# Optimization experiments

Hardware: AMD Instinct MI355X
Metric: run time of the kernel (lower is better)

## Reference

```python
import jax, jax.numpy as jnp
import numpy as np

TAU = 2.0
EPS_G = 1e-10   # gumbel numerical eps
EPS_H = 1e-12   # entropy log eps


def _gumbel(u):
    # u ~ Uniform(0,1) -> standard Gumbel noise
    return -jnp.log(-jnp.log(u + EPS_G) + EPS_G)


def setup_inputs() -> dict:
    key = jax.random.key(0)
    k1, k2, k3, k4 = jax.random.split(key, 4)
    B, T, D, K = 4, 1024, 512, 8192
    x = jax.random.normal(k1, (B, T, D), dtype=jnp.float32)
    codebook = jax.random.normal(k2, (K, D), dtype=jnp.float32)
    u1 = jax.random.uniform(k3, (B * T, K), dtype=jnp.float32)
    u2 = jax.random.uniform(k4, (B * T, K), dtype=jnp.float32)
    return {"x": x, "codebook": codebook, "u1": u1, "u2": u2}


def reference(x, codebook, u1, u2):
    B, T, D = x.shape
    x_flat = x.reshape(-1, D)                                  # (N, D)
    x_sq = jnp.sum(x_flat * x_flat, axis=1, keepdims=True)     # (N, 1)
    c_sq = jnp.sum(codebook * codebook, axis=1)                # (K,)
    xc = x_flat @ codebook.T                                   # (N, K)
    logits = -(x_sq + c_sq - 2.0 * xc)                         # -||x - c||^2

    # soft gumbel-softmax (first independent noise draw)
    probs_soft = jax.nn.softmax((logits + _gumbel(u1)) / TAU, axis=-1)  # (N, K)
    quantized_soft = (probs_soft @ codebook).reshape(B, T, D)

    # hard gumbel-softmax indices (second independent noise draw);
    # argmax of the hard one-hot == argmax of perturbed logits
    indices = jnp.argmax(logits + _gumbel(u2), axis=-1).reshape(B, T)

    codebook_loss = jnp.mean((quantized_soft - jax.lax.stop_gradient(x)) ** 2)
    enc_commitment_loss = jnp.mean((x - jax.lax.stop_gradient(quantized_soft)) ** 2)

    entropy = -jnp.sum(probs_soft * jnp.log(probs_soft + EPS_H), axis=1)  # (N,)
    mean_entropy = jnp.mean(entropy)

    return quantized_soft, indices, codebook_loss, enc_commitment_loss, mean_entropy
```

## Files before the change

kernel.cpp:

```cpp
#include <hip/hip_runtime.h>
#include <math.h>

#define NROWS 4096
#define KCODES 8192
#define DDIM 512
#define IDX_OFF 2097152
#define L0_OFF  2101248
#define L1_OFF  2101249
#define ENT_OFF 2101250
#define ARGMAX_MARGIN 0.05f
#define FIX_CHUNK 256
#define FIX_CPR (KCODES / FIX_CHUNK)

#define TOP2_UPD(v1, k1, v2, k2, h, k)                                 \
    do {                                                               \
        if ((h) > (v1)) { v2 = v1; k2 = k1; v1 = (h); k1 = (k); }      \
        else if ((h) > (v2)) { v2 = (h); k2 = (k); }                   \
    } while (0)

typedef __attribute__((ext_vector_type(8))) short bf16x8;
typedef __attribute__((ext_vector_type(4))) float f32x4;

__device__ __forceinline__ float gumbelfast(float u) {
    float a = __logf(u + 1e-10f);
    float b = __logf(1e-10f - a);
    return -b;
}
__device__ __forceinline__ ushort f2bf(float f) {
    uint u = __float_as_uint(f);
    return (ushort)((u + 0x7FFFu + ((u >> 16) & 1u)) >> 16);
}
__device__ __forceinline__ float bf2f(ushort h) {
    return __uint_as_float(((uint)h) << 16);
}

__device__ __forceinline__ float np_log32(float x) {
    return (float)log((double)x);
}
__device__ __forceinline__ float np_gumbel(float u) {
    float a  = __fadd_rn(u, 1e-10f);
    float la = np_log32(a);
    float b  = __fadd_rn(-la, 1e-10f);
    float lb = np_log32(b);
    return -lb;
}
__device__ float np_sumsq512(const float* __restrict__ a) {
    float blk[4];
    #pragma unroll
    for (int b = 0; b < 4; ++b) {
        const float* p = a + b * 128;
        float r[8];
        #pragma unroll
        for (int j = 0; j < 8; ++j) r[j] = __fmul_rn(p[j], p[j]);
        for (int i = 8; i < 128; i += 8) {
            #pragma unroll
            for (int j = 0; j < 8; ++j)
                r[j] = __fadd_rn(r[j], __fmul_rn(p[i + j], p[i + j]));
        }
        blk[b] = __fadd_rn(__fadd_rn(__fadd_rn(r[0], r[1]), __fadd_rn(r[2], r[3])),
                           __fadd_rn(__fadd_rn(r[4], r[5]), __fadd_rn(r[6], r[7])));
    }
    return __fadd_rn(__fadd_rn(blk[0], blk[1]), __fadd_rn(blk[2], blk[3]));
}

__device__ __forceinline__ float dot4(float4 a, float4 b) {
    return a.x*b.x + a.y*b.y + a.z*b.z + a.w*b.w;
}
__device__ __forceinline__ void fma4(float4& o, float p, float4 c) {
    o.x += p*c.x; o.y += p*c.y; o.z += p*c.z; o.w += p*c.w;
}

__global__ __launch_bounds__(256) void vq_csq(const float* __restrict__ cb,
                                              float* __restrict__ csq,
                                              int* __restrict__ flag_cnt) {
    if (blockIdx.x == 0 && threadIdx.x == 0) flag_cnt[0] = 0;
    int row = blockIdx.x * 256 + threadIdx.x;
    if (row < KCODES) csq[row] = np_sumsq512(cb + (size_t)row * DDIM);
}

__global__ __launch_bounds__(256) void vq_fixup(
        const float* __restrict__ x, const float* __restrict__ cb,
        const float* __restrict__ u2, const float* __restrict__ csq,
        const int* __restrict__ flag_cnt, const int* __restrict__ flag_rows,
        float* __restrict__ out) {
    __shared__ float xrow[DDIM];
    __shared__ float bv[4];
    __shared__ int   bk[4];
    const int n = flag_cnt[0];
    for (int w = blockIdx.x; w < n; w += gridDim.x) {
        const int row = flag_rows[w];
        for (int i = threadIdx.x; i < DDIM; i += 256)
            xrow[i] = x[(size_t)row * DDIM + i];
        __syncthreads();
        const float xsq = np_sumsq512(xrow);
        float best = -1e30f; int bidx = 0x7fffffff;
        for (int k = threadIdx.x; k < KCODES; k += 256) {
            const float* c = cb + (size_t)k * DDIM;
            float acc1 = 0.f, acc2 = 0.f;
            #pragma unroll 8
            for (int d = 0; d < 384; ++d) acc1 = fmaf(xrow[d], c[d], acc1);
            #pragma unroll 8
            for (int d = 384; d < DDIM; ++d) acc2 = fmaf(xrow[d], c[d], acc2);
            float xc = __fadd_rn(acc1, acc2);
            float t1 = __fadd_rn(xsq, csq[k]);
            float t2 = __fmul_rn(2.0f, xc);
            float t3 = __fsub_rn(t1, t2);
            float logit = -t3;
            float h = __fadd_rn(logit, np_gumbel(u2[(size_t)row * KCODES + k]));
            if (h > best || (h == best && k < bidx)) { best = h; bidx = k; }
        }
        const int lane = threadIdx.x & 63, wv = threadIdx.x >> 6;
        #pragma unroll
        for (int m = 32; m >= 1; m >>= 1) {
            float ov = __shfl_xor(best, m); int ok = __shfl_xor(bidx, m);
            if (ov > best || (ov == best && ok < bidx)) { best = ov; bidx = ok; }
        }
        if (lane == 0) { bv[wv] = best; bk[wv] = bidx; }
        __syncthreads();
        if (threadIdx.x == 0) {
            float b = bv[0]; int bi = bk[0];
            #pragma unroll
            for (int i = 1; i < 4; ++i)
                if (bv[i] > b || (bv[i] == b && bk[i] < bi)) { b = bv[i]; bi = bk[i]; }
            out[IDX_OFF + row] = (float)bi;
        }
        __syncthreads();
    }
}

__global__ __launch_bounds__(256) void vq_fixup2(
        const float* __restrict__ x, const float* __restrict__ cb,
        const float* __restrict__ u2, const float* __restrict__ csq,
        const int* __restrict__ flag_cnt, const int* __restrict__ flag_rows,
        unsigned long long* __restrict__ packed) {
    __shared__ float xrow[DDIM];
    __shared__ float xsq_sh;
    __shared__ unsigned long long redp[4];
    const int n = flag_cnt[0];
    const int total = n * FIX_CPR;
    for (int item = blockIdx.x; item < total; item += gridDim.x) {
        const int w = item / FIX_CPR;
        const int chunk = item - w * FIX_CPR;
        const int row = flag_rows[w];
        __syncthreads();
        for (int i = threadIdx.x; i < DDIM; i += 256)
            xrow[i] = x[(size_t)row * DDIM + i];
        __syncthreads();
        if (threadIdx.x == 0) xsq_sh = np_sumsq512(xrow);
        __syncthreads();
        const float xsq = xsq_sh;
        const int k = chunk * FIX_CHUNK + threadIdx.x;
        const float* c = cb + (size_t)k * DDIM;
        float acc1 = 0.f, acc2 = 0.f;
        #pragma unroll 8
        for (int d = 0; d < 384; ++d) acc1 = fmaf(xrow[d], c[d], acc1);
        #pragma unroll 8
        for (int d = 384; d < DDIM; ++d) acc2 = fmaf(xrow[d], c[d], acc2);
        float xc = __fadd_rn(acc1, acc2);
        float t1 = __fadd_rn(xsq, csq[k]);
        float t2 = __fmul_rn(2.0f, xc);
        float logit = -__fsub_rn(t1, t2);
        float h = __fadd_rn(logit, np_gumbel(u2[(size_t)row * KCODES + k]));
        uint hb = __float_as_uint(h);
        uint key = (hb & 0x80000000u) ? ~hb : (hb | 0x80000000u);
        unsigned long long val = ((unsigned long long)key << 32)
                               | (unsigned long long)(0xFFFFFFFFu - (uint)k);
        #pragma unroll
        for (int m = 32; m >= 1; m >>= 1) {
            unsigned long long o = __shfl_xor(val, m);
            if (o > val) val = o;
        }
        if ((threadIdx.x & 63) == 0) redp[threadIdx.x >> 6] = val;
        __syncthreads();
        if (threadIdx.x == 0) {
            unsigned long long v = redp[0];
            if (redp[1] > v) v = redp[1];
            if (redp[2] > v) v = redp[2];
            if (redp[3] > v) v = redp[3];
            atomicMax(&packed[row], v);
        }
    }
}


__global__ __launch_bounds__(256) void vq_split(const float4* __restrict__ in,
                                                ushort* __restrict__ hi,
                                                ushort* __restrict__ lo) {
    int i = blockIdx.x * 256 + threadIdx.x;
    float4 v = in[i];
    ushort4 h, l;
    h.x = f2bf(v.x); h.y = f2bf(v.y); h.z = f2bf(v.z); h.w = f2bf(v.w);
    l.x = f2bf(v.x - bf2f(h.x)); l.y = f2bf(v.y - bf2f(h.y));
    l.z = f2bf(v.z - bf2f(h.z)); l.w = f2bf(v.w - bf2f(h.w));
    ((ushort4*)hi)[i] = h;
    ((ushort4*)lo)[i] = l;
}

__global__ __launch_bounds__(256) void vq_trans(const float* __restrict__ cb,
                                                ushort* __restrict__ cbT) {
    __shared__ ushort T[64][65];
    const int k0 = blockIdx.x * 64, d0 = blockIdx.y * 64;
    const int lane = threadIdx.x & 63, w = threadIdx.x >> 6;
    #pragma unroll
    for (int i = 0; i < 16; ++i) {
        int ky = i * 4 + w;
        float f = cb[(size_t)(k0 + ky) * DDIM + d0 + lane];
        T[lane][ky] = f2bf(f);
    }
    __syncthreads();
    #pragma unroll
    for (int i = 0; i < 16; ++i) {
        int dy = i * 4 + w;
        cbT[(size_t)(d0 + dy) * KCODES + k0 + lane] = T[dy][lane];
    }
}

__global__ __launch_bounds__(256) void vq_gemm1(
        const ushort* __restrict__ xhi, const ushort* __restrict__ xlo,
        const ushort* __restrict__ chi, const ushort* __restrict__ clo,
        const float* __restrict__ csq, float* __restrict__ S0) {
    __shared__ short As[2][128 * 72];
    __shared__ short Bs[2][128 * 72];
    const int tid = threadIdx.x;
    const int lane = tid & 63, wid = tid >> 6;
    const int wr = wid >> 1, wc = wid & 1;
    const int m0 = blockIdx.y * 128, n0 = blockIdx.x * 128;

    f32x4 acc[4][4] = {};
    for (int kk = 0; kk < 8; ++kk) {
        const int k0 = kk * 64;
        __syncthreads();
        #pragma unroll
        for (int i = 0; i < 4; ++i) {
            int c = tid + i * 256;
            int row = c >> 3, off = (c & 7) * 8;
            int lidx = row * 72 + off;
            size_t gA = (size_t)(m0 + row) * DDIM + k0 + off;
            size_t gB = (size_t)(n0 + row) * DDIM + k0 + off;
            *(bf16x8*)&As[0][lidx] = *(const bf16x8*)(xhi + gA);
            *(bf16x8*)&As[1][lidx] = *(const bf16x8*)(xlo + gA);
            *(bf16x8*)&Bs[0][lidx] = *(const bf16x8*)(chi + gB);
            *(bf16x8*)&Bs[1][lidx] = *(const bf16x8*)(clo + gB);
        }
        __syncthreads();
        #pragma unroll
        for (int ks = 0; ks < 2; ++ks) {
            const int ko = ks * 32 + (lane >> 4) * 8;
            bf16x8 ah[4], al[4], bh[4], bl[4];
            #pragma unroll
            for (int m = 0; m < 4; ++m) {
                int r = wr * 64 + m * 16 + (lane & 15);
                ah[m] = *(bf16x8*)&As[0][r * 72 + ko];
                al[m] = *(bf16x8*)&As[1][r * 72 + ko];
            }
            #pragma unroll
            for (int n = 0; n < 4; ++n) {
                int r = wc * 64 + n * 16 + (lane & 15);
                bh[n] = *(bf16x8*)&Bs[0][r * 72 + ko];
                bl[n] = *(bf16x8*)&Bs[1][r * 72 + ko];
            }
            #pragma unroll
            for (int m = 0; m < 4; ++m)
                #pragma unroll
                for (int n = 0; n < 4; ++n) {
                    acc[m][n] = __builtin_amdgcn_mfma_f32_16x16x32_bf16(ah[m], bh[n], acc[m][n], 0, 0, 0);
                    acc[m][n] = __builtin_amdgcn_mfma_f32_16x16x32_bf16(ah[m], bl[n], acc[m][n], 0, 0, 0);
                    acc[m][n] = __builtin_amdgcn_mfma_f32_16x16x32_bf16(al[m], bh[n], acc[m][n], 0, 0, 0);
                }
        }
    }
    #pragma unroll
    for (int n = 0; n < 4; ++n) {
        int col = n0 + wc * 64 + n * 16 + (lane & 15);
        float cq = csq[col];
        #pragma unroll
        for (int m = 0; m < 4; ++m) {
            int rbase = m0 + wr * 64 + m * 16 + ((lane >> 4) << 2);
            #pragma unroll
            for (int j = 0; j < 4; ++j)
                S0[(size_t)(rbase + j) * KCODES + col] = 2.0f * acc[m][n][j] - cq;
        }
    }
}

__global__ __launch_bounds__(1024) void vq_soft(
        float* __restrict__ S0, const float* __restrict__ u1,
        const float* __restrict__ u2,
        float* __restrict__ Aarr, float* __restrict__ entarr,
        float* __restrict__ out, int* __restrict__ flag_cnt,
        int* __restrict__ flag_rows, unsigned long long* __restrict__ packed) {
    __shared__ float redm[16], redA[16], redB[16];
    __shared__ float rv1[16], rv2[16];
    __shared__ int   rk1[16], rk2[16];
    const int row = blockIdx.x, tid = threadIdx.x;
    const int lane = tid & 63, wid = tid >> 6;
    const size_t base = (size_t)row * KCODES;
    if (tid == 0) packed[row] = 0ULL;

    const int ka = tid * 4;
    const int kb = 4096 + tid * 4;
    float4 Sa = *(const float4*)(S0 + base + ka);
    float4 Sb = *(const float4*)(S0 + base + kb);
    float4 Ua = *(const float4*)(u1 + base + ka);
    float4 Ub = *(const float4*)(u1 + base + kb);
    float4 Va = *(const float4*)(u2 + base + ka);
    float4 Vb = *(const float4*)(u2 + base + kb);

    float v1 = -1e30f, v2 = -1e30f; int k1 = 0x7fffffff, k2 = 0x7fffffff;
    float h;
    h = Sa.x + gumbelfast(Va.x); TOP2_UPD(v1, k1, v2, k2, h, ka);
    h = Sa.y + gumbelfast(Va.y); TOP2_UPD(v1, k1, v2, k2, h, ka + 1);
    h = Sa.z + gumbelfast(Va.z); TOP2_UPD(v1, k1, v2, k2, h, ka + 2);
    h = Sa.w + gumbelfast(Va.w); TOP2_UPD(v1, k1, v2, k2, h, ka + 3);
    h = Sb.x + gumbelfast(Vb.x); TOP2_UPD(v1, k1, v2, k2, h, kb);
    h = Sb.y + gumbelfast(Vb.y); TOP2_UPD(v1, k1, v2, k2, h, kb + 1);
    h = Sb.z + gumbelfast(Vb.z); TOP2_UPD(v1, k1, v2, k2, h, kb + 2);
    h = Sb.w + gumbelfast(Vb.w); TOP2_UPD(v1, k1, v2, k2, h, kb + 3);

    float4 sa, sb;
    sa.x = (Sa.x + gumbelfast(Ua.x)) * 0.5f;
    sa.y = (Sa.y + gumbelfast(Ua.y)) * 0.5f;
    sa.z = (Sa.z + gumbelfast(Ua.z)) * 0.5f;
    sa.w = (Sa.w + gumbelfast(Ua.w)) * 0.5f;
    sb.x = (Sb.x + gumbelfast(Ub.x)) * 0.5f;
    sb.y = (Sb.y + gumbelfast(Ub.y)) * 0.5f;
    sb.z = (Sb.z + gumbelfast(Ub.z)) * 0.5f;
    sb.w = (Sb.w + gumbelfast(Ub.w)) * 0.5f;
    float mloc = fmaxf(fmaxf(fmaxf(sa.x, sa.y), fmaxf(sa.z, sa.w)),
                       fmaxf(fmaxf(sb.x, sb.y), fmaxf(sb.z, sb.w)));
    #pragma unroll
    for (int m = 32; m >= 1; m >>= 1) mloc = fmaxf(mloc, __shfl_xor(mloc, m));
    if (lane == 0) redm[wid] = mloc;
    __syncthreads();
    float mrow = redm[0];
    #pragma unroll
    for (int i = 1; i < 16; ++i) mrow = fmaxf(mrow, redm[i]);

    float A, Be;
    {
        float d0 = sa.x - mrow, d1 = sa.y - mrow, d2 = sa.z - mrow, d3 = sa.w - mrow;
        float e0 = __expf(d0), e1 = __expf(d1), e2 = __expf(d2), e3 = __expf(d3);
        float d4 = sb.x - mrow, d5 = sb.y - mrow, d6 = sb.z - mrow, d7 = sb.w - mrow;
        float e4 = __expf(d4), e5 = __expf(d5), e6 = __expf(d6), e7 = __expf(d7);
        A  = (((e0 + e1) + e2) + e3) + ((((e4 + e5) + e6) + e7));
        Be = (((e0*d0 + e1*d1) + e2*d2) + e3*d3) + ((((e4*d4 + e5*d5) + e6*d6) + e7*d7));
        ushort* Prow = (ushort*)(S0 + base);
        ushort4 pa, pb;
        pa.x = f2bf(e0); pa.y = f2bf(e1); pa.z = f2bf(e2); pa.w = f2bf(e3);
        pb.x = f2bf(e4); pb.y = f2bf(e5); pb.z = f2bf(e6); pb.w = f2bf(e7);
        *(ushort4*)(Prow + ka) = pa;
        *(ushort4*)(Prow + kb) = pb;
    }
    #pragma unroll
    for (int m = 32; m >= 1; m >>= 1) { A += __shfl_xor(A, m); Be += __shfl_xor(Be, m); }
    #pragma unroll
    for (int m = 32; m >= 1; m >>= 1) {
        float ov1 = __shfl_xor(v1, m); int ok1 = __shfl_xor(k1, m);
        float ov2 = __shfl_xor(v2, m); int ok2 = __shfl_xor(k2, m);
        if (ov1 > v1 || (ov1 == v1 && ok1 < k1)) {
            float nv2; int nk2;
            if (v1 > ov2 || (v1 == ov2 && k1 < ok2)) { nv2 = v1; nk2 = k1; }
            else { nv2 = ov2; nk2 = ok2; }
            v1 = ov1; k1 = ok1; v2 = nv2; k2 = nk2;
        } else if (ov1 > v2 || (ov1 == v2 && ok1 < k2)) { v2 = ov1; k2 = ok1; }
    }
    if (lane == 0) {
        redA[wid] = A; redB[wid] = Be;
        rv1[wid] = v1; rv2[wid] = v2; rk1[wid] = k1; rk2[wid] = k2;
    }
    __syncthreads();
    if (tid == 0) {
        float At = 0.f, Bt = 0.f;
        #pragma unroll
        for (int i = 0; i < 16; ++i) { At += redA[i]; Bt += redB[i]; }
        float V1 = rv1[0], V2 = rv2[0]; int K1 = rk1[0], K2 = rk2[0];
        #pragma unroll
        for (int i = 1; i < 16; ++i) {
            float ov1 = rv1[i], ov2 = rv2[i]; int ok1 = rk1[i], ok2 = rk2[i];
            if (ov1 > V1 || (ov1 == V1 && ok1 < K1)) {
                float nv2; int nk2;
                if (V1 > ov2 || (V1 == ov2 && K1 < ok2)) { nv2 = V1; nk2 = K1; }
                else { nv2 = ov2; nk2 = ok2; }
                V1 = ov1; K1 = ok1; V2 = nv2; K2 = nk2;
            } else if (ov1 > V2 || (ov1 == V2 && ok1 < K2)) { V2 = ov1; K2 = ok1; }
        }
        Aarr[row] = At;
        entarr[row] = logf(At) - Bt / At;
        out[IDX_OFF + row] = (float)K1;
        if (V1 - V2 < ARGMAX_MARGIN) {
            int s = atomicAdd(flag_cnt, 1);
            flag_rows[s] = row;
        }
    }
}

#define G2_BK 128
__global__ __launch_bounds__(512) void vq_gemm2b(
        const ushort* __restrict__ P, const ushort* __restrict__ cbT,
        const float* __restrict__ Aarr, const float* __restrict__ x,
        float* __restrict__ out, float* __restrict__ wloss) {
    __shared__ short Ap[2][128 * 136];
    __shared__ short Bt[2][64 * 136];
    __shared__ float redl[8];
    const int tid = threadIdx.x;
    const int lane = tid & 63, wid = tid >> 6;
    const int wr = wid & 3, wc = wid >> 2;
    const int bid = blockIdx.x;
    const int mblk = bid & 31, nblk = bid >> 5;
    const int m0 = mblk * 128, n0 = nblk * 64;

    bf16x8 rp[4], rb[2];
    f32x4 acc[2][2] = {};

    #define G2_LOAD(t)                                                         \
        do {                                                                   \
            const int k0_ = (t) * G2_BK;                                       \
            _Pragma("unroll")                                                  \
            for (int i = 0; i < 4; ++i) {                                      \
                int c = tid + i * 512;                                         \
                int row = c >> 4, off = (c & 15) * 8;                          \
                rp[i] = *(const bf16x8*)(P + (size_t)(m0 + row) * 16384 + k0_ + off); \
            }                                                                  \
            _Pragma("unroll")                                                  \
            for (int i = 0; i < 2; ++i) {                                      \
                int c = tid + i * 512;                                         \
                int row = c >> 4, off = (c & 15) * 8;                          \
                rb[i] = *(const bf16x8*)(cbT + (size_t)(n0 + row) * 8192 + k0_ + off); \
            }                                                                  \
        } while (0)

    #define G2_WRITE(buf)                                                      \
        do {                                                                   \
            _Pragma("unroll")                                                  \
            for (int i = 0; i < 4; ++i) {                                      \
                int c = tid + i * 512;                                         \
                int row = c >> 4, off = (c & 15) * 8;                          \
                *(bf16x8*)&Ap[buf][row * 136 + off] = rp[i];                   \
            }                                                                  \
            _Pragma("unroll")                                                  \
            for (int i = 0; i < 2; ++i) {                                      \
                int c = tid + i * 512;                                         \
                int row = c >> 4, off = (c & 15) * 8;                          \
                *(bf16x8*)&Bt[buf][row * 136 + off] = rb[i];                   \
            }                                                                  \
        } while (0)

    G2_LOAD(0);
    G2_WRITE(0);
    __syncthreads();
    int cur = 0;
    for (int t = 0; t < KCODES / G2_BK; ++t) {
        if (t < KCODES / G2_BK - 1) G2_LOAD(t + 1);
        #pragma unroll
        for (int ks = 0; ks < 4; ++ks) {
            const int ko = ks * 32 + (lane >> 4) * 8;
            bf16x8 af[2], bfr[2];
            #pragma unroll
            for (int m = 0; m < 2; ++m)
                af[m] = *(bf16x8*)&Ap[cur][(wr * 32 + m * 16 + (lane & 15)) * 136 + ko];
            #pragma unroll
            for (int n = 0; n < 2; ++n)
                bfr[n] = *(bf16x8*)&Bt[cur][(wc * 32 + n * 16 + (lane & 15)) * 136 + ko];
            #pragma unroll
            for (int m = 0; m < 2; ++m)
                #pragma unroll
                for (int n = 0; n < 2; ++n)
                    acc[m][n] = __builtin_amdgcn_mfma_f32_16x16x32_bf16(af[m], bfr[n], acc[m][n], 0, 0, 0);
        }
        if (t < KCODES / G2_BK - 1) {
            __syncthreads();
            G2_WRITE(cur ^ 1);
            __syncthreads();
            cur ^= 1;
        }
    }
    #undef G2_LOAD
    #undef G2_WRITE

    float lsum = 0.f;
    #pragma unroll
    for (int n = 0; n < 2; ++n) {
        int col = n0 + wc * 32 + n * 16 + (lane & 15);
        #pragma unroll
        for (int m = 0; m < 2; ++m) {
            int rbase = m0 + wr * 32 + m * 16 + ((lane >> 4) << 2);
            #pragma unroll
            for (int j = 0; j < 4; ++j) {
                int row = rbase + j;
                float inva = 1.0f / Aarr[row];
                float q = acc[m][n][j] * inva;
                out[(size_t)row * DDIM + col] = q;
                float d = q - x[(size_t)row * DDIM + col];
                lsum += d * d;
            }
        }
    }
    #pragma unroll
    for (int m = 32; m >= 1; m >>= 1) lsum += __shfl_xor(lsum, m);
    if (lane == 0) redl[wid] = lsum;
    __syncthreads();
    if (tid == 0) {
        float s = 0.f;
        #pragma unroll
        for (int i = 0; i < 8; ++i) s += redl[i];
        wloss[bid] = s;
    }
}

__global__ __launch_bounds__(256) void vq_finalize2(
        const float* __restrict__ wloss, const float* __restrict__ entarr,
        const int* __restrict__ flag_cnt, const int* __restrict__ flag_rows,
        const unsigned long long* __restrict__ packed, float* __restrict__ out) {
    __shared__ float redl[4], rede[4];
    int tid = threadIdx.x;
    const int n = flag_cnt[0];
    for (int w = tid; w < n; w += 256) {
        int row = flag_rows[w];
        uint lowbits = (uint)(packed[row] & 0xFFFFFFFFULL);
        out[IDX_OFF + row] = (float)(0xFFFFFFFFu - lowbits);
    }
    float l = wloss[tid];
    float e = 0.f;
    #pragma unroll
    for (int i = 0; i < 16; ++i) e += entarr[tid + i * 256];
    #pragma unroll
    for (int m = 32; m >= 1; m >>= 1) { l += __shfl_xor(l, m); e += __shfl_xor(e, m); }
    if ((tid & 63) == 0) { redl[tid >> 6] = l; rede[tid >> 6] = e; }
    __syncthreads();
    if (tid == 0) {
        float L = (((redl[0] + redl[1]) + redl[2]) + redl[3]) * (1.0f / 2097152.0f);
        float E = (((rede[0] + rede[1]) + rede[2]) + rede[3]) * (1.0f / 4096.0f);
        out[L0_OFF]  = L;
        out[L1_OFF]  = L;
        out[ENT_OFF] = E;
    }
}

#define BR 16
#define KT 128
#define NUM_KT 64
#define NUM_DC 4

__device__ __forceinline__ float gumbelf(float u) {
    return -logf(-logf(u + 1e-10f) + 1e-10f);
}

__global__ __launch_bounds__(256) void vq_main_fb(
        const float* __restrict__ x, const float* __restrict__ cb,
        const float* __restrict__ u1, const float* __restrict__ u2,
        const float* __restrict__ csq, float* __restrict__ out,
        float* __restrict__ wloss, float* __restrict__ went,
        int* __restrict__ flag_cnt, int* __restrict__ flag_rows) {
    __shared__ float4 Xs[BR][129];
    __shared__ float4 Cs[KT * 32];
    __shared__ float4 Ol[BR][128];
    __shared__ float4 Ps[BR][32];
    __shared__ float  xsq_s[BR];
    __shared__ float  f_s[BR];
    __shared__ float  A_s[BR];
    __shared__ float  ent_s[BR];
    __shared__ float  red4[4];

    const int tid = threadIdx.x;
    const int rg  = tid >> 5;
    const int cg  = tid & 31;
    const int r0  = rg * 2;
    const int r1  = r0 + 1;
    const int row0g = blockIdx.x * BR;
    const float4* cb4 = (const float4*)cb;

    {
        const float4* xg = (const float4*)x + (size_t)row0g * 128;
        #pragma unroll
        for (int i = 0; i < 8; ++i) {
            int idx = tid + i * 256;
            int r = idx >> 7, q = idx & 127;
            Xs[r][q] = xg[r * 128 + q];
            Ol[r][q] = make_float4(0.f, 0.f, 0.f, 0.f);
        }
    }
    __syncthreads();
    {
        int r = tid >> 4, part = tid & 15;
        float s = 0.f;
        #pragma unroll
        for (int q = 0; q < 8; ++q) {
            float4 v = Xs[r][part * 8 + q];
            s += v.x*v.x + v.y*v.y + v.z*v.z + v.w*v.w;
        }
        #pragma unroll
        for (int m = 8; m >= 1; m >>= 1) s += __shfl_xor(s, m);
        if (part == 0) xsq_s[r] = s;
    }
    __syncthreads();
    const float xsq0 = xsq_s[r0];
    const float xsq1 = xsq_s[r1];

    float m0 = -1e30f, m1 = -1e30f;
    float A0 = 0.f, A1 = 0.f;
    float B0 = 0.f, B1 = 0.f;
    float hb0 = -1e30f, hb1 = -1e30f;
    float hc0 = -1e30f, hc1 = -1e30f;
    int   kb0 = 0, kb1 = 0, kc0 = 0, kc1 = 0;

    for (int t = 0; t < NUM_KT; ++t) {
        const int ktb = t * KT;
        float a00=0.f,a01=0.f,a02=0.f,a03=0.f,a10=0.f,a11=0.f,a12=0.f,a13=0.f;

        for (int dc = 0; dc < NUM_DC; ++dc) {
            #pragma unroll
            for (int i = 0; i < 16; ++i) {
                int idx = tid + i * 256;
                int k = idx >> 5, q = idx & 31;
                Cs[k * 32 + (q ^ ((k >> 2) & 7))] =
                    cb4[(size_t)(ktb + k) * 128 + dc * 32 + q];
            }
            __syncthreads();
            const int qb = dc * 32;
            const int c4 = cg * 4;
            #pragma unroll 4
            for (int dd = 0; dd < 32; ++dd) {
                float4 xv0 = Xs[r0][qb + dd];
                float4 xv1 = Xs[r1][qb + dd];
                int swq = dd ^ (cg & 7);
                float4 cv0 = Cs[(c4 + 0) * 32 + swq];
                float4 cv1 = Cs[(c4 + 1) * 32 + swq];
                float4 cv2 = Cs[(c4 + 2) * 32 + swq];
                float4 cv3 = Cs[(c4 + 3) * 32 + swq];
                a00 += dot4(xv0, cv0); a01 += dot4(xv0, cv1);
                a02 += dot4(xv0, cv2); a03 += dot4(xv0, cv3);
                a10 += dot4(xv1, cv0); a11 += dot4(xv1, cv1);
                a12 += dot4(xv1, cv2); a13 += dot4(xv1, cv3);
            }
            __syncthreads();
        }
        {
            const int kg0 = ktb + cg * 4;
            size_t ur0 = (size_t)(row0g + r0) * KCODES + kg0;
            size_t ur1 = (size_t)(row0g + r1) * KCODES + kg0;
            float4 u1a = *(const float4*)(u1 + ur0);
            float4 u1b = *(const float4*)(u1 + ur1);
            float4 u2a = *(const float4*)(u2 + ur0);
            float4 u2b = *(const float4*)(u2 + ur1);
            float cs0 = csq[kg0], cs1 = csq[kg0+1], cs2 = csq[kg0+2], cs3 = csq[kg0+3];
            {
                float l0 = 2.f*a00 - xsq0 - cs0;
                float l1 = 2.f*a01 - xsq0 - cs1;
                float l2 = 2.f*a02 - xsq0 - cs2;
                float l3 = 2.f*a03 - xsq0 - cs3;
                float h;
                h = l0 + gumbelf(u2a.x); TOP2_UPD(hb0, kb0, hc0, kc0, h, kg0);
                h = l1 + gumbelf(u2a.y); TOP2_UPD(hb0, kb0, hc0, kc0, h, kg0+1);
                h = l2 + gumbelf(u2a.z); TOP2_UPD(hb0, kb0, hc0, kc0, h, kg0+2);
                h = l3 + gumbelf(u2a.w); TOP2_UPD(hb0, kb0, hc0, kc0, h, kg0+3);
                float s0 = (l0 + gumbelf(u1a.x)) * 0.5f;
                float s1 = (l1 + gumbelf(u1a.y)) * 0.5f;
                float s2 = (l2 + gumbelf(u1a.z)) * 0.5f;
                float s3 = (l3 + gumbelf(u1a.w)) * 0.5f;
                float tmax = fmaxf(fmaxf(s0, s1), fmaxf(s2, s3));
                #pragma unroll
                for (int m = 16; m >= 1; m >>= 1) tmax = fmaxf(tmax, __shfl_xor(tmax, m));
                float mn = fmaxf(m0, tmax);
                float p0 = expf(s0 - mn), p1 = expf(s1 - mn);
                float p2 = expf(s2 - mn), p3 = expf(s3 - mn);
                float tA = p0 + p1 + p2 + p3;
                float tB = p0*(s0-mn) + p1*(s1-mn) + p2*(s2-mn) + p3*(s3-mn);
                #pragma unroll
                for (int m = 16; m >= 1; m >>= 1) { tA += __shfl_xor(tA, m); tB += __shfl_xor(tB, m); }
                float f = expf(m0 - mn);
                B0 = f * (B0 + (m0 - mn) * A0) + tB;
                A0 = f * A0 + tA;
                m0 = mn;
                Ps[r0][cg] = make_float4(p0, p1, p2, p3);
                if (cg == 0) f_s[r0] = f;
            }
            {
                float l0 = 2.f*a10 - xsq1 - cs0;
                float l1 = 2.f*a11 - xsq1 - cs1;
                float l2 = 2.f*a12 - xsq1 - cs2;
                float l3 = 2.f*a13 - xsq1 - cs3;
                float h;
                h = l0 + gumbelf(u2b.x); TOP2_UPD(hb1, kb1, hc1, kc1, h, kg0);
                h = l1 + gumbelf(u2b.y); TOP2_UPD(hb1, kb1, hc1, kc1, h, kg0+1);
                h = l2 + gumbelf(u2b.z); TOP2_UPD(hb1, kb1, hc1, kc1, h, kg0+2);
                h = l3 + gumbelf(u2b.w); TOP2_UPD(hb1, kb1, hc1, kc1, h, kg0+3);
                float s0 = (l0 + gumbelf(u1b.x)) * 0.5f;
                float s1 = (l1 + gumbelf(u1b.y)) * 0.5f;
                float s2 = (l2 + gumbelf(u1b.z)) * 0.5f;
                float s3 = (l3 + gumbelf(u1b.w)) * 0.5f;
                float tmax = fmaxf(fmaxf(s0, s1), fmaxf(s2, s3));
                #pragma unroll
                for (int m = 16; m >= 1; m >>= 1) tmax = fmaxf(tmax, __shfl_xor(tmax, m));
                float mn = fmaxf(m1, tmax);
                float p0 = expf(s0 - mn), p1 = expf(s1 - mn);
                float p2 = expf(s2 - mn), p3 = expf(s3 - mn);
                float tA = p0 + p1 + p2 + p3;
                float tB = p0*(s0-mn) + p1*(s1-mn) + p2*(s2-mn) + p3*(s3-mn);
                #pragma unroll
                for (int m = 16; m >= 1; m >>= 1) { tA += __shfl_xor(tA, m); tB += __shfl_xor(tB, m); }
                float f = expf(m1 - mn);
                B1 = f * (B1 + (m1 - mn) * A1) + tB;
                A1 = f * A1 + tA;
                m1 = mn;
                Ps[r1][cg] = make_float4(p0, p1, p2, p3);
                if (cg == 0) f_s[r1] = f;
            }
        }
        __syncthreads();

        for (int dc = 0; dc < NUM_DC; ++dc) {
            #pragma unroll
            for (int i = 0; i < 16; ++i) {
                int idx = tid + i * 256;
                int k = idx >> 5, q = idx & 31;
                Cs[k * 32 + (q ^ ((k >> 2) & 7))] =
                    cb4[(size_t)(ktb + k) * 128 + dc * 32 + q];
            }
            __syncthreads();
            float4 o0 = make_float4(0.f,0.f,0.f,0.f);
            float4 o1 = make_float4(0.f,0.f,0.f,0.f);
            #pragma unroll 2
            for (int k4 = 0; k4 < 32; ++k4) {
                float4 pv0 = Ps[r0][k4];
                float4 pv1 = Ps[r1][k4];
                int sq = cg ^ (k4 & 7);
                float4 cva = Cs[(k4*4 + 0) * 32 + sq];
                float4 cvb = Cs[(k4*4 + 1) * 32 + sq];
                float4 cvc = Cs[(k4*4 + 2) * 32 + sq];
                float4 cvd = Cs[(k4*4 + 3) * 32 + sq];
                fma4(o0, pv0.x, cva); fma4(o0, pv0.y, cvb);
                fma4(o0, pv0.z, cvc); fma4(o0, pv0.w, cvd);
                fma4(o1, pv1.x, cva); fma4(o1, pv1.y, cvb);
                fma4(o1, pv1.z, cvc); fma4(o1, pv1.w, cvd);
            }
            float fr0 = f_s[r0], fr1 = f_s[r1];
            int oq = dc * 32 + cg;
            float4 Ov0 = Ol[r0][oq];
            Ov0.x = Ov0.x*fr0 + o0.x; Ov0.y = Ov0.y*fr0 + o0.y;
            Ov0.z = Ov0.z*fr0 + o0.z; Ov0.w = Ov0.w*fr0 + o0.w;
            Ol[r0][oq] = Ov0;
            float4 Ov1 = Ol[r1][oq];
            Ov1.x = Ov1.x*fr1 + o1.x; Ov1.y = Ov1.y*fr1 + o1.y;
            Ov1.z = Ov1.z*fr1 + o1.z; Ov1.w = Ov1.w*fr1 + o1.w;
            Ol[r1][oq] = Ov1;
            __syncthreads();
        }
    }
    {
        float ent0 = logf(A0) - B0 / A0;
        float v1 = hb0, v2 = hc0; int k1 = kb0, k2 = kc0;
        #pragma unroll
        for (int m = 16; m >= 1; m >>= 1) {
            float ov1 = __shfl_xor(v1, m); int ok1 = __shfl_xor(k1, m);
            float ov2 = __shfl_xor(v2, m); int ok2 = __shfl_xor(k2, m);
            if (ov1 > v1 || (ov1 == v1 && ok1 < k1)) {
                float nv2; int nk2;
                if (v1 > ov2 || (v1 == ov2 && k1 < ok2)) { nv2 = v1; nk2 = k1; }
                else { nv2 = ov2; nk2 = ok2; }
                v1 = ov1; k1 = ok1; v2 = nv2; k2 = nk2;
            } else if (ov1 > v2 || (ov1 == v2 && ok1 < k2)) {
                v2 = ov1; k2 = ok1;
            }
        }
        if (cg == 0) {
            out[IDX_OFF + row0g + r0] = (float)k1;
            if (v1 - v2 < ARGMAX_MARGIN) {
                int s = atomicAdd(flag_cnt, 1);
                flag_rows[s] = row0g + r0;
            }
            ent_s[r0] = ent0;
            A_s[r0] = A0;
        }
        float ent1 = logf(A1) - B1 / A1;
        v1 = hb1; v2 = hc1; k1 = kb1; k2 = kc1;
        #pragma unroll
        for (int m = 16; m >= 1; m >>= 1) {
            float ov1 = __shfl_xor(v1, m); int ok1 = __shfl_xor(k1, m);
            float ov2 = __shfl_xor(v2, m); int ok2 = __shfl_xor(k2, m);
            if (ov1 > v1 || (ov1 == v1 && ok1 < k1)) {
                float nv2; int nk2;
                if (v1 > ov2 || (v1 == ov2 && k1 < ok2)) { nv2 = v1; nk2 = k1; }
                else { nv2 = ov2; nk2 = ok2; }
                v1 = ov1; k1 = ok1; v2 = nv2; k2 = nk2;
            } else if (ov1 > v2 || (ov1 == v2 && ok1 < k2)) {
                v2 = ov1; k2 = ok1;
            }
        }
        if (cg == 0) {
            out[IDX_OFF + row0g + r1] = (float)k1;
            if (v1 - v2 < ARGMAX_MARGIN) {
                int s = atomicAdd(flag_cnt, 1);
                flag_rows[s] = row0g + r1;
            }
            ent_s[r1] = ent1;
            A_s[r1] = A1;
        }
    }
    __syncthreads();

    float lsum = 0.f;
    float4* outq = (float4*)out;
    #pragma unroll
    for (int i = 0; i < 8; ++i) {
        int idx = tid + i * 256;
        int r = idx >> 7, q = idx & 127;
        float inva = 1.f / A_s[r];
        float4 Ov = Ol[r][q];
        float4 qv = make_float4(Ov.x*inva, Ov.y*inva, Ov.z*inva, Ov.w*inva);
        outq[(size_t)(row0g + r) * 128 + q] = qv;
        float4 xv = Xs[r][q];
        float dx;
        dx = qv.x - xv.x; lsum += dx*dx;
        dx = qv.y - xv.y; lsum += dx*dx;
        dx = qv.z - xv.z; lsum += dx*dx;
        dx = qv.w - xv.w; lsum += dx*dx;
    }
    #pragma unroll
    for (int m = 32; m >= 1; m >>= 1) lsum += __shfl_xor(lsum, m);
    if ((tid & 63) == 0) red4[tid >> 6] = lsum;
    __syncthreads();
    if (tid == 0) {
        wloss[blockIdx.x] = red4[0] + red4[1] + red4[2] + red4[3];
        float es = 0.f;
        for (int r = 0; r < BR; ++r) es += ent_s[r];
        went[blockIdx.x] = es;
    }
}

__global__ __launch_bounds__(256) void vq_finalize_fb(const float* __restrict__ wloss,
                                                      const float* __restrict__ went,
                                                      float* __restrict__ out) {
    __shared__ float redl[4], rede[4];
    int tid = threadIdx.x;
    float l = wloss[tid];
    float e = went[tid];
    #pragma unroll
    for (int m = 32; m >= 1; m >>= 1) { l += __shfl_xor(l, m); e += __shfl_xor(e, m); }
    if ((tid & 63) == 0) { redl[tid >> 6] = l; rede[tid >> 6] = e; }
    __syncthreads();
    if (tid == 0) {
        float L = (redl[0] + redl[1] + redl[2] + redl[3]) * (1.0f / 2097152.0f);
        float E = (rede[0] + rede[1] + rede[2] + rede[3]) * (1.0f / 4096.0f);
        out[L0_OFF]  = L;
        out[L1_OFF]  = L;
        out[ENT_OFF] = E;
    }
}

extern "C" void kernel_launch(void* const* d_in, const int* in_sizes, int n_in,
                              void* d_out, int out_size, void* d_ws, size_t ws_size,
                              hipStream_t stream) {
    const float* x  = (const float*)d_in[0];
    const float* cb = (const float*)d_in[1];
    const float* u1 = (const float*)d_in[2];
    const float* u2 = (const float*)d_in[3];
    float* out = (float*)d_out;

    const size_t NEED = 0xA018000ULL;
    if (ws_size >= NEED) {
        char* w = (char*)d_ws;
        float*  S0   = (float*)w;
        ushort* xhi  = (ushort*)(w + 0x8000000);
        ushort* xlo  = (ushort*)(w + 0x8400000);
        ushort* chi  = (ushort*)(w + 0x8800000);
        ushort* clo  = (ushort*)(w + 0x9000000);
        ushort* cbT  = (ushort*)(w + 0x9800000);
        float*  csq  = (float*)(w + 0xA000000);
        float*  Aarr = (float*)(w + 0xA008000);
        float*  enta = (float*)(w + 0xA00C000);
        float*  wlp  = (float*)(w + 0xA010000);
        int*    fcnt = (int*)(w + 0xA010400);
        int*    frws = (int*)(w + 0xA010800);
        unsigned long long* packed = (unsigned long long*)(w + 0x8000000);

        vq_csq<<<KCODES / 256, 256, 0, stream>>>(cb, csq, fcnt);
        vq_split<<<2048, 256, 0, stream>>>((const float4*)x, xhi, xlo);
        vq_split<<<4096, 256, 0, stream>>>((const float4*)cb, chi, clo);
        vq_trans<<<dim3(128, 8), 256, 0, stream>>>(cb, cbT);
        vq_gemm1<<<dim3(64, 32), 256, 0, stream>>>(xhi, xlo, chi, clo, csq, S0);
        vq_soft<<<NROWS, 1024, 0, stream>>>(S0, u1, u2, Aarr, enta, out, fcnt, frws, packed);
        vq_gemm2b<<<256, 512, 0, stream>>>((const ushort*)S0, cbT, Aarr, x, out, wlp);
        vq_fixup2<<<1024, 256, 0, stream>>>(x, cb, u2, csq, fcnt, frws, packed);
        vq_finalize2<<<1, 256, 0, stream>>>(wlp, enta, fcnt, frws, packed, out);
    } else {
        float* ws  = (float*)d_ws;
        float* csq    = ws;
        float* wlossp = ws + KCODES;
        float* wentp  = ws + KCODES + 256;
        int*   fcnt   = (int*)(ws + KCODES + 512);
        int*   frows  = fcnt + 1;

        vq_csq<<<KCODES / 256, 256, 0, stream>>>(cb, csq, fcnt);
        vq_main_fb<<<NROWS / BR, 256, 0, stream>>>(x, cb, u1, u2, csq, out,
                                                   wlossp, wentp, fcnt, frows);
        vq_fixup<<<256, 256, 0, stream>>>(x, cb, u2, csq, fcnt, frows, out);
        vq_finalize_fb<<<1, 256, 0, stream>>>(wlossp, wentp, out);
    }
}
```

Before: 377.9 us.

## Prefetch GEMM1 tiles into registers, fuse codebook prep, parallelize norm kernel

The first GEMM now loads the next K-slice of the hi/lo bf16 tiles into registers while the MFMAs run on the current shared-memory tile, then writes it to LDS between barriers. This hides global-load latency behind compute. The codebook hi/lo split is folded into the transpose kernel so the codebook is read once for all three outputs, removing a launch. The codebook-norm kernel uses 32 threads per row with a shuffle reduction instead of one thread per row, which changes the summation order slightly. The prefetch adds register pressure and the fused prep kernel does scalar 2-byte stores.

```diff
diff --git a/kernel.cpp b/kernel.cpp
--- a/kernel.cpp
+++ b/kernel.cpp
@@ -70,12 +70,27 @@
     o.x += p*c.x; o.y += p*c.y; o.z += p*c.z; o.w += p*c.w;
 }
 
-__global__ __launch_bounds__(256) void vq_csq(const float* __restrict__ cb,
-                                              float* __restrict__ csq,
-                                              int* __restrict__ flag_cnt) {
+__global__ __launch_bounds__(256) void vq_csq2(const float* __restrict__ cb,
+                                               float* __restrict__ csq,
+                                               int* __restrict__ flag_cnt) {
     if (blockIdx.x == 0 && threadIdx.x == 0) flag_cnt[0] = 0;
-    int row = blockIdx.x * 256 + threadIdx.x;
-    if (row < KCODES) csq[row] = np_sumsq512(cb + (size_t)row * DDIM);
+    const int tid = threadIdx.x;
+    const int row = blockIdx.x * 8 + (tid >> 5);
+    const int rl  = tid & 31;
+    const int b   = rl >> 3, j = rl & 7;
+    const float* p = cb + (size_t)row * DDIM + b * 128 + j;
+    float r = __fmul_rn(p[0], p[0]);
+    #pragma unroll
+    for (int i = 1; i < 16; ++i) {
+        float v = p[i * 8];
+        r = __fadd_rn(r, __fmul_rn(v, v));
+    }
+    r = __fadd_rn(r, __shfl_xor(r, 1));
+    r = __fadd_rn(r, __shfl_xor(r, 2));
+    r = __fadd_rn(r, __shfl_xor(r, 4));
+    r = __fadd_rn(r, __shfl_xor(r, 8));
+    r = __fadd_rn(r, __shfl_xor(r, 16));
+    if (rl == 0) csq[row] = r;
 }
 
 __global__ __launch_bounds__(256) void vq_fixup(
@@ -196,16 +211,22 @@
     ((ushort4*)lo)[i] = l;
 }
 
-__global__ __launch_bounds__(256) void vq_trans(const float* __restrict__ cb,
-                                                ushort* __restrict__ cbT) {
+__global__ __launch_bounds__(256) void vq_prep_cb(const float* __restrict__ cb,
+                                                  ushort* __restrict__ chi,
+                                                  ushort* __restrict__ clo,
+                                                  ushort* __restrict__ cbT) {
     __shared__ ushort T[64][65];
     const int k0 = blockIdx.x * 64, d0 = blockIdx.y * 64;
     const int lane = threadIdx.x & 63, w = threadIdx.x >> 6;
     #pragma unroll
     for (int i = 0; i < 16; ++i) {
         int ky = i * 4 + w;
-        float f = cb[(size_t)(k0 + ky) * DDIM + d0 + lane];
-        T[lane][ky] = f2bf(f);
+        size_t g = (size_t)(k0 + ky) * DDIM + d0 + lane;
+        float f = cb[g];
+        ushort h = f2bf(f);
+        chi[g] = h;
+        clo[g] = f2bf(f - bf2f(h));
+        T[lane][ky] = h;
     }
     __syncthreads();
     #pragma unroll
@@ -226,23 +247,44 @@
     const int wr = wid >> 1, wc = wid & 1;
     const int m0 = blockIdx.y * 128, n0 = blockIdx.x * 128;
 
+    bf16x8 sAh[4], sAl[4], sBh[4], sBl[4];
     f32x4 acc[4][4] = {};
+
+    #define G1_LOAD(kkv)                                                       \
+        do {                                                                   \
+            const int k0_ = (kkv) * 64;                                        \
+            _Pragma("unroll")                                                  \
+            for (int i = 0; i < 4; ++i) {                                      \
+                int c = tid + i * 256;                                         \
+                int row = c >> 3, off = (c & 7) * 8;                           \
+                size_t gA = (size_t)(m0 + row) * DDIM + k0_ + off;             \
+                size_t gB = (size_t)(n0 + row) * DDIM + k0_ + off;             \
+                sAh[i] = *(const bf16x8*)(xhi + gA);                           \
+                sAl[i] = *(const bf16x8*)(xlo + gA);                           \
+                sBh[i] = *(const bf16x8*)(chi + gB);                           \
+                sBl[i] = *(const bf16x8*)(clo + gB);                           \
+            }                                                                  \
+        } while (0)
+
+    #define G1_WRITE()                                                         \
+        do {                                                                   \
+            _Pragma("unroll")                                                  \
+            for (int i = 0; i < 4; ++i) {                                      \
+                int c = tid + i * 256;                                         \
+                int row = c >> 3, off = (c & 7) * 8;                           \
+                int lidx = row * 72 + off;                                     \
+                *(bf16x8*)&As[0][lidx] = sAh[i];                               \
+                *(bf16x8*)&As[1][lidx] = sAl[i];                               \
+                *(bf16x8*)&Bs[0][lidx] = sBh[i];                               \
+                *(bf16x8*)&Bs[1][lidx] = sBl[i];                               \
+            }                                                                  \
+        } while (0)
+
+    G1_LOAD(0);
+    G1_WRITE();
+    __syncthreads();
     for (int kk = 0; kk < 8; ++kk) {
-        const int k0 = kk * 64;
-        __syncthreads();
-        #pragma unroll
-        for (int i = 0; i < 4; ++i) {
-            int c = tid + i * 256;
-            int row = c >> 3, off = (c & 7) * 8;
-            int lidx = row * 72 + off;
-            size_t gA = (size_t)(m0 + row) * DDIM + k0 + off;
-            size_t gB = (size_t)(n0 + row) * DDIM + k0 + off;
-            *(bf16x8*)&As[0][lidx] = *(const bf16x8*)(xhi + gA);
-            *(bf16x8*)&As[1][lidx] = *(const bf16x8*)(xlo + gA);
-            *(bf16x8*)&Bs[0][lidx] = *(const bf16x8*)(chi + gB);
-            *(bf16x8*)&Bs[1][lidx] = *(const bf16x8*)(clo + gB);
-        }
-        __syncthreads();
+        if (kk < 7) G1_LOAD(kk + 1);
         #pragma unroll
         for (int ks = 0; ks < 2; ++ks) {
             const int ko = ks * 32 + (lane >> 4) * 8;
@@ -268,7 +310,15 @@
                     acc[m][n] = __builtin_amdgcn_mfma_f32_16x16x32_bf16(al[m], bh[n], acc[m][n], 0, 0, 0);
                 }
         }
-    }
+        if (kk < 7) {
+            __syncthreads();
+            G1_WRITE();
+            __syncthreads();
+        }
+    }
+    #undef G1_LOAD
+    #undef G1_WRITE
+
     #pragma unroll
     for (int n = 0; n < 4; ++n) {
         int col = n0 + wc * 64 + n * 16 + (lane & 15);
@@ -873,10 +923,9 @@
         int*    frws = (int*)(w + 0xA010800);
         unsigned long long* packed = (unsigned long long*)(w + 0x8000000);
 
-        vq_csq<<<KCODES / 256, 256, 0, stream>>>(cb, csq, fcnt);
+        vq_csq2<<<KCODES / 8, 256, 0, stream>>>(cb, csq, fcnt);
         vq_split<<<2048, 256, 0, stream>>>((const float4*)x, xhi, xlo);
-        vq_split<<<4096, 256, 0, stream>>>((const float4*)cb, chi, clo);
-        vq_trans<<<dim3(128, 8), 256, 0, stream>>>(cb, cbT);
+        vq_prep_cb<<<dim3(128, 8), 256, 0, stream>>>(cb, chi, clo, cbT);
         vq_gemm1<<<dim3(64, 32), 256, 0, stream>>>(xhi, xlo, chi, clo, csq, S0);
         vq_soft<<<NROWS, 1024, 0, stream>>>(S0, u1, u2, Aarr, enta, out, fcnt, frws, packed);
         vq_gemm2b<<<256, 512, 0, stream>>>((const ushort*)S0, cbT, Aarr, x, out, wlp);
@@ -890,7 +939,7 @@
         int*   fcnt   = (int*)(ws + KCODES + 512);
         int*   frows  = fcnt + 1;
 
-        vq_csq<<<KCODES / 256, 256, 0, stream>>>(cb, csq, fcnt);
+        vq_csq2<<<KCODES / 8, 256, 0, stream>>>(cb, csq, fcnt);
         vq_main_fb<<<NROWS / BR, 256, 0, stream>>>(x, cb, u1, u2, csq, out,
                                                    wlossp, wentp, fcnt, frows);
         vq_fixup<<<256, 256, 0, stream>>>(x, cb, u2, csq, fcnt, frows, out);
```

New measurement: 367.5 us, median of 2. 1.03x faster.
